# Optimization experiments

Hardware: AMD Instinct MI355X
Metric: run time of the kernel (lower is better)

The kernel has to match this reference:

```python
import jax, jax.numpy as jnp
import numpy as np

B, S, D = 8, 4096, 256
NUM_WINDOW = 8
WIN = S // NUM_WINDOW          # 512
H = 2                          # num_heads
K = D                          # key_dim = d_model per source
DFF = 1024
LN_EPS = 1e-3                  # keras LayerNormalization default epsilon


def _layer_norm(x, g, b):
    mu = jnp.mean(x, axis=-1, keepdims=True)
    var = jnp.mean(jnp.square(x - mu), axis=-1, keepdims=True)
    return (x - mu) * jax.lax.rsqrt(var + LN_EPS) * g + b


def setup_inputs() -> dict:
    key = jax.random.key(0)
    ks = jax.random.split(key, 12)
    s = 0.02
    inp = {
        "x": jax.random.normal(ks[0], (B, S, D), dtype=jnp.float32),
        # MHA projections (keras MultiHeadAttention layout)
        "Wq": jax.random.normal(ks[1], (D, H, K), dtype=jnp.float32) * s,
        "bq": jnp.zeros((H, K), dtype=jnp.float32),
        "Wk": jax.random.normal(ks[2], (D, H, K), dtype=jnp.float32) * s,
        "bk": jnp.zeros((H, K), dtype=jnp.float32),
        "Wv": jax.random.normal(ks[3], (D, H, K), dtype=jnp.float32) * s,
        "bv": jnp.zeros((H, K), dtype=jnp.float32),
        "Wo": jax.random.normal(ks[4], (H, K, D), dtype=jnp.float32) * s,
        "bo": jnp.zeros((D,), dtype=jnp.float32),
        "ln1_g": jnp.ones((D,), dtype=jnp.float32),
        "ln1_b": jnp.zeros((D,), dtype=jnp.float32),
        # FeedForward
        "W1": jax.random.normal(ks[5], (D, DFF), dtype=jnp.float32) * s,
        "b1": jnp.zeros((DFF,), dtype=jnp.float32),
        "W2": jax.random.normal(ks[6], (DFF, D), dtype=jnp.float32) * s,
        "b2": jnp.zeros((D,), dtype=jnp.float32),
        "ln2_g": jnp.ones((D,), dtype=jnp.float32),
        "ln2_b": jnp.zeros((D,), dtype=jnp.float32),
    }
    return inp


def reference(x, Wq, bq, Wk, bk, Wv, bv, Wo, bo, ln1_g, ln1_b,
              W1, b1, W2, b2, ln2_g, ln2_b):
    # --- Localized self-attention: block-diagonal over NUM_WINDOW windows ---
    xw = x.reshape(B, NUM_WINDOW, WIN, D)               # [b, w, s, d]
    q = jnp.einsum('bwsd,dhk->bwshk', xw, Wq) + bq      # [b, w, s, h, k]
    k = jnp.einsum('bwsd,dhk->bwshk', xw, Wk) + bk
    v = jnp.einsum('bwsd,dhk->bwshk', xw, Wv) + bv
    scores = jnp.einsum('bwshk,bwthk->bwhst', q, k) / jnp.sqrt(
        jnp.asarray(K, dtype=x.dtype))                  # [b, w, h, s, t]
    attn = jax.nn.softmax(scores, axis=-1)
    ctx = jnp.einsum('bwhst,bwthk->bwshk', attn, v)     # [b, w, s, h, k]
    attn_out = jnp.einsum('bwshk,hkd->bwsd', ctx, Wo) + bo
    attn_out = attn_out.reshape(B, S, D)                # concat over windows
    x = _layer_norm(x + attn_out, ln1_g, ln1_b)
    # --- FeedForward (dropout inactive at inference) ---
    h = jax.nn.relu(x @ W1 + b1)
    ff = h @ W2 + b2
    return _layer_norm(x + ff, ln2_g, ln2_b)
```

## Files before the change

### kernel.cpp

```cpp
#include <hip/hip_runtime.h>

typedef unsigned short u16;
typedef short short8 __attribute__((ext_vector_type(8)));
typedef float f32x4 __attribute__((ext_vector_type(4)));

#define AS1C const __attribute__((address_space(1))) void*
#define AS3P __attribute__((address_space(3))) void*

__device__ __forceinline__ u16 f2b(float f) {
  unsigned u = __float_as_uint(f);
  return (u16)((u + 0x7fffu + ((u >> 16) & 1u)) >> 16);
}
__device__ __forceinline__ float b2f(u16 h) {
  return __uint_as_float((unsigned)h << 16);
}

#define BB 8
#define SS 4096
#define DD 256
#define MTOK (BB*SS)

#define OFF_WQKVT  ((size_t)0)
#define OFF_WOT    ((size_t)786432)
#define OFF_W1T    ((size_t)1048576)
#define OFF_W2T    ((size_t)1572864)
#define OFF_BQKV   ((size_t)2097152)
#define OFF_XB     ((size_t)2103296)
#define OFF_QKV    ((size_t)18880512)
#define OFF_YB     ((size_t)52434944)
#define OFF_HB     ((size_t)69212160)
#define OFF_VT     ((size_t)119543808)
#define OFF_CTX    ((size_t)153098240)

__global__ __launch_bounds__(256) void cast_x_kernel(const float* __restrict__ x,
                                                     u16* __restrict__ xb) {
  size_t i = ((size_t)blockIdx.x * 256 + threadIdx.x) * 4;
  float4 v = *(const float4*)(x + i);
  ushort4 o;
  o.x = f2b(v.x); o.y = f2b(v.y); o.z = f2b(v.z); o.w = f2b(v.w);
  *(ushort4*)(xb + i) = o;
}

__global__ __launch_bounds__(256) void prep_w_kernel(
    const float* __restrict__ Wq, const float* __restrict__ Wk, const float* __restrict__ Wv,
    const float* __restrict__ Wo, const float* __restrict__ W1, const float* __restrict__ W2,
    const float* __restrict__ bq, const float* __restrict__ bk, const float* __restrict__ bv,
    u16* __restrict__ wqkvt, u16* __restrict__ wot, u16* __restrict__ w1t,
    u16* __restrict__ w2t, float* __restrict__ bqkv)
{
  for (int i = blockIdx.x * 256 + threadIdx.x; i < 1050112; i += 1024 * 256) {
    if (i < 393216) {
      int n = i >> 8, d = i & 255;
      const float* W = (n < 512) ? Wq : (n < 1024) ? Wk : Wv;
      int nn = n & 511;
      wqkvt[i] = f2b(W[d * 512 + nn]);
    } else if (i < 524288) {
      int j = i - 393216;
      int dout = j >> 9, hk = j & 511;
      wot[j] = f2b(Wo[hk * 256 + dout]);
    } else if (i < 786432) {
      int j = i - 524288;
      int f = j >> 8, d = j & 255;
      w1t[j] = f2b(W1[d * 1024 + f]);
    } else if (i < 1048576) {
      int j = i - 786432;
      int d = j >> 10, f = j & 1023;
      w2t[j] = f2b(W2[f * 256 + d]);
    } else {
      int n = i - 1048576;
      bqkv[n] = (n < 512) ? bq[n] : (n < 1024) ? bk[n - 512] : bv[n - 1024];
    }
  }
}

__global__ __launch_bounds__(256) void gemm_nres(
    const u16* __restrict__ A, const u16* __restrict__ BT,
    const float* __restrict__ bias, u16* __restrict__ C,
    u16* __restrict__ vt, int N, int vbase, int relu)
{
  __shared__ __align__(16) u16 lds[16384];
  const int tid = threadIdx.x, lane = tid & 63, wid = tid >> 6;
  const int ln = lane & 15, quad = lane >> 4;
  const int pn = blockIdx.x >> 5;
  const int mg = blockIdx.x & 31;
  const int wno = (wid >> 1) << 5;
  const int wmo = (wid & 1) << 4;
  const long mbase = (long)mg << 10;
  const int nb = pn << 6;
  const u16* Bp = BT + (size_t)nb * 256;
  const u16* Ap = A + (size_t)mbase * 256;

#pragma unroll
  for (int p = 0; p < 8; p++) {
    const int s = p * 256 + tid;
    const int row = s >> 5, pc = s & 31;
    const int c = pc ^ (row & 31);
    __builtin_amdgcn_global_load_lds(
        (AS1C)(Bp + (size_t)row * 256 + c * 8), (AS3P)(lds + s * 8), 16, 0, 0);
  }
  __syncthreads();
  short8 breg[2][8];
#pragma unroll
  for (int j = 0; j < 2; j++) {
    const int row = wno + j * 16 + ln;
#pragma unroll
    for (int ks = 0; ks < 8; ks++)
      breg[j][ks] = *(const short8*)(lds + row * 256 + (((ks << 2) + quad) ^ (row & 31)) * 8);
  }
  __syncthreads();

#pragma unroll
  for (int p = 0; p < 4; p++) {
    const int s = p * 256 + tid;
    const int row = s >> 5, pc = s & 31;
    const int c = pc ^ (row & 31);
    __builtin_amdgcn_global_load_lds(
        (AS1C)(Ap + (size_t)row * 256 + c * 8), (AS3P)(lds + s * 8), 16, 0, 0);
  }

  for (int it = 0; it < 32; it++) {
    const int cur = it & 1;
    const u16* Ab = lds + cur * 8192;
    __syncthreads();
    if (it + 1 < 32) {
      const u16* An = Ap + (size_t)(it + 1) * 32 * 256;
      u16* Ax = lds + (cur ^ 1) * 8192;
#pragma unroll
      for (int p = 0; p < 4; p++) {
        const int s = p * 256 + tid;
        const int row = s >> 5, pc = s & 31;
        const int c = pc ^ (row & 31);
        __builtin_amdgcn_global_load_lds(
            (AS1C)(An + (size_t)row * 256 + c * 8), (AS3P)(Ax + s * 8), 16, 0, 0);
      }
    }
    f32x4 acc[2];
    acc[0] = (f32x4){0.f, 0.f, 0.f, 0.f};
    acc[1] = (f32x4){0.f, 0.f, 0.f, 0.f};
    const int r0 = wmo + ln;
#pragma unroll
    for (int ks = 0; ks < 8; ks++) {
      const short8 a0 = *(const short8*)(Ab + r0 * 256 + (((ks << 2) + quad) ^ (r0 & 31)) * 8);
      acc[0] = __builtin_amdgcn_mfma_f32_16x16x32_bf16(breg[0][ks], a0, acc[0], 0, 0, 0);
      acc[1] = __builtin_amdgcn_mfma_f32_16x16x32_bf16(breg[1][ks], a0, acc[1], 0, 0, 0);
    }
    const long m = mbase + it * 32 + wmo + ln;
    if (nb < vbase) {
#pragma unroll
      for (int j = 0; j < 2; j++) {
        const int n0 = nb + wno + j * 16 + quad * 4;
        f32x4 v = acc[j];
        const float4 b4 = *(const float4*)(bias + n0);
        v[0] += b4.x; v[1] += b4.y; v[2] += b4.z; v[3] += b4.w;
        if (relu) {
#pragma unroll
          for (int r = 0; r < 4; r++) v[r] = fmaxf(v[r], 0.f);
        }
        ushort4 ob;
        ob.x = f2b(v[0]); ob.y = f2b(v[1]); ob.z = f2b(v[2]); ob.w = f2b(v[3]);
        *(ushort4*)(C + (size_t)m * N + n0) = ob;
      }
    } else {
      const int bw = (int)(m >> 9), t = (int)(m & 511);
#pragma unroll
      for (int j = 0; j < 2; j++) {
        const int n0 = nb + wno + j * 16 + quad * 4;
        const int rel = n0 - vbase;
        const int h = rel >> 8, k0 = rel & 255;
        u16* vp = vt + (size_t)(bw * 2 + h) * 131072 + (size_t)k0 * 512 + t;
        const float4 b4 = *(const float4*)(bias + n0);
        vp[0]    = f2b(acc[j][0] + b4.x);
        vp[512]  = f2b(acc[j][1] + b4.y);
        vp[1024] = f2b(acc[j][2] + b4.z);
        vp[1536] = f2b(acc[j][3] + b4.w);
      }
    }
  }
}

__global__ __launch_bounds__(512, 4) void attn_fused(const u16* __restrict__ qkv,
                                                     const u16* __restrict__ vt,
                                                     u16* __restrict__ ctx)
{
  __shared__ __align__(16) u16 lds[35328];
  const int tid = threadIdx.x, lane = tid & 63, wid = tid >> 6;
  const int ln = lane & 15, quad = lane >> 4;
  const int bat = blockIdx.x & 127, mt = blockIdx.x >> 7;
  const int bw = bat >> 1, h = bat & 1;
  const u16* Qb = qkv + (size_t)bw * 786432 + (size_t)h * 256 + (size_t)(mt * 64) * 1536;
  const u16* Kb = qkv + (size_t)bw * 786432 + 512 + (size_t)h * 256;
  const u16* Vb = vt + (size_t)bat * 131072;
  const int wn = wid * 64;
  const int wno = wid * 32;
  u16* Pbuf = lds;
  float* red1 = (float*)(lds + 33280);
  float* red2 = red1 + 512;

  const u16* qp[4];
  const u16* kp[4];
#pragma unroll
  for (int i = 0; i < 4; i++) qp[i] = Qb + (size_t)(i * 16 + ln) * 1536 + quad * 8;
#pragma unroll
  for (int j = 0; j < 4; j++) kp[j] = Kb + (size_t)(wn + j * 16 + ln) * 1536 + quad * 8;

  f32x4 acc[4][4];
#pragma unroll
  for (int i = 0; i < 4; i++)
#pragma unroll
    for (int j = 0; j < 4; j++) acc[i][j] = (f32x4){0.f, 0.f, 0.f, 0.f};

#pragma unroll
  for (int ki = 0; ki < 8; ki++) {
    const int kt = ki * 32;
    short8 a[4], b[4];
#pragma unroll
    for (int i = 0; i < 4; i++) a[i] = *(const short8*)(qp[i] + kt);
#pragma unroll
    for (int j = 0; j < 4; j++) b[j] = *(const short8*)(kp[j] + kt);
    __builtin_amdgcn_s_setprio(1);
#pragma unroll
    for (int i = 0; i < 4; i++)
#pragma unroll
      for (int j = 0; j < 4; j++)
        acc[i][j] = __builtin_amdgcn_mfma_f32_16x16x32_bf16(b[j], a[i], acc[i][j], 0, 0, 0);
    __builtin_amdgcn_s_setprio(0);
  }

  float rowmax[4], rowsum[4];
#pragma unroll
  for (int i = 0; i < 4; i++) {
    float m = -1e30f;
#pragma unroll
    for (int j = 0; j < 4; j++)
#pragma unroll
      for (int r = 0; r < 4; r++) m = fmaxf(m, acc[i][j][r]);
    m = fmaxf(m, __shfl_xor(m, 16));
    m = fmaxf(m, __shfl_xor(m, 32));
    if (quad == 0) red1[wid * 64 + i * 16 + ln] = m;
  }
  __syncthreads();
#pragma unroll
  for (int i = 0; i < 4; i++) {
    float m = -1e30f;
#pragma unroll
    for (int w = 0; w < 8; w++) m = fmaxf(m, red1[w * 64 + i * 16 + ln]);
    rowmax[i] = m;
  }
#pragma unroll
  for (int i = 0; i < 4; i++) {
    float s = 0.f;
#pragma unroll
    for (int j = 0; j < 4; j++)
#pragma unroll
      for (int r = 0; r < 4; r++) {
        const float e = __expf((acc[i][j][r] - rowmax[i]) * 0.0625f);
        acc[i][j][r] = e; s += e;
      }
    s += __shfl_xor(s, 16);
    s += __shfl_xor(s, 32);
    if (quad == 0) red2[wid * 64 + i * 16 + ln] = s;
  }
  __syncthreads();
#pragma unroll
  for (int i = 0; i < 4; i++) {
    float s = 0.f;
#pragma unroll
    for (int w = 0; w < 8; w++) s += red2[w * 64 + i * 16 + ln];
    rowsum[i] = 1.f / s;
  }

  short8 vC[2][2], vN[2][2];
#pragma unroll
  for (int j = 0; j < 2; j++) {
    const int kV = wno + j * 16 + ln;
#pragma unroll
    for (int ks = 0; ks < 2; ks++)
      vC[j][ks] = *(const short8*)(Vb + (size_t)kV * 512 + (ks * 4 + quad) * 8);
  }

#pragma unroll
  for (int i = 0; i < 4; i++)
#pragma unroll
    for (int j = 0; j < 4; j++) {
      ushort4 pb;
      pb.x = f2b(acc[i][j][0] * rowsum[i]);
      pb.y = f2b(acc[i][j][1] * rowsum[i]);
      pb.z = f2b(acc[i][j][2] * rowsum[i]);
      pb.w = f2b(acc[i][j][3] * rowsum[i]);
      *(ushort4*)(Pbuf + (i * 16 + ln) * 520 + wn + j * 16 + quad * 4) = pb;
    }
  __syncthreads();

  f32x4 o[4][2];
#pragma unroll
  for (int i = 0; i < 4; i++) {
    o[i][0] = (f32x4){0.f, 0.f, 0.f, 0.f};
    o[i][1] = (f32x4){0.f, 0.f, 0.f, 0.f};
  }

#pragma unroll
  for (int c = 0; c < 8; c++) {
    if (c < 7) {
#pragma unroll
      for (int j = 0; j < 2; j++) {
        const int kV = wno + j * 16 + ln;
#pragma unroll
        for (int ks = 0; ks < 2; ks++)
          vN[j][ks] = *(const short8*)(Vb + (size_t)kV * 512 + (c + 1) * 64 + (ks * 4 + quad) * 8);
      }
    }
    __builtin_amdgcn_s_setprio(1);
#pragma unroll
    for (int ks = 0; ks < 2; ks++) {
      short8 ap[4];
#pragma unroll
      for (int i = 0; i < 4; i++)
        ap[i] = *(const short8*)(Pbuf + (i * 16 + ln) * 520 + c * 64 + ks * 32 + quad * 8);
#pragma unroll
      for (int j = 0; j < 2; j++)
#pragma unroll
        for (int i = 0; i < 4; i++)
          o[i][j] = __builtin_amdgcn_mfma_f32_16x16x32_bf16(vC[j][ks], ap[i], o[i][j], 0, 0, 0);
    }
    __builtin_amdgcn_s_setprio(0);
#pragma unroll
    for (int j = 0; j < 2; j++)
#pragma unroll
      for (int ks = 0; ks < 2; ks++) vC[j][ks] = vN[j][ks];
  }

  const size_t tokr0 = (size_t)bw * 512 + mt * 64;
#pragma unroll
  for (int i = 0; i < 4; i++) {
    const size_t row = tokr0 + i * 16 + ln;
#pragma unroll
    for (int j = 0; j < 2; j++) {
      const int col = h * 256 + wno + j * 16 + quad * 4;
      ushort4 ob;
      ob.x = f2b(o[i][j][0]); ob.y = f2b(o[i][j][1]);
      ob.z = f2b(o[i][j][2]); ob.w = f2b(o[i][j][3]);
      *(ushort4*)(ctx + row * 512 + col) = ob;
    }
  }
}

__global__ __launch_bounds__(256) void gemm_ln(
    const u16* __restrict__ A, const u16* __restrict__ BT,
    const float* __restrict__ bias, const u16* __restrict__ residb,
    const float* __restrict__ g, const float* __restrict__ beta,
    float* __restrict__ yout, u16* __restrict__ ybout, int K)
{
  __shared__ __align__(16) u16 As[2][2048];
  __shared__ __align__(16) u16 Bs[2][8192];
  __shared__ float redS[4][64], redQ[4][64];
  const int tid = threadIdx.x, lane = tid & 63, wid = tid >> 6;
  const int ln = lane & 15, quad = lane >> 4;
  const long bm = (long)blockIdx.x * 64;
  const int wn = wid * 64;
  const u16* Ab = A + (size_t)bm * K;
  const int nk = K >> 5;

  f32x4 acc[4][4];
#pragma unroll
  for (int i = 0; i < 4; i++)
#pragma unroll
    for (int j = 0; j < 4; j++) acc[i][j] = (f32x4){0.f, 0.f, 0.f, 0.f};

  {
    const int row = tid >> 2, c = tid & 3;
    __builtin_amdgcn_global_load_lds(
        (AS1C)(Ab + (size_t)row * K + c * 8), (AS3P)(&As[0][0] + tid * 8), 16, 0, 0);
#pragma unroll
    for (int p = 0; p < 4; p++) {
      const int s = p * 256 + tid;
      const int br = s >> 2, bc = s & 3;
      __builtin_amdgcn_global_load_lds(
          (AS1C)(BT + (size_t)br * K + bc * 8), (AS3P)(&Bs[0][0] + s * 8), 16, 0, 0);
    }
  }

  for (int kti = 0; kti < nk; kti++) {
    const int cur = kti & 1;
    __syncthreads();
    if (kti + 1 < nk) {
      const int kt = (kti + 1) * 32, nxt = cur ^ 1;
      const int row = tid >> 2, c = tid & 3;
      __builtin_amdgcn_global_load_lds(
          (AS1C)(Ab + (size_t)row * K + kt + c * 8), (AS3P)(&As[nxt][0] + tid * 8), 16, 0, 0);
#pragma unroll
      for (int p = 0; p < 4; p++) {
        const int s = p * 256 + tid;
        const int br = s >> 2, bc = s & 3;
        __builtin_amdgcn_global_load_lds(
            (AS1C)(BT + (size_t)br * K + kt + bc * 8), (AS3P)(&Bs[nxt][0] + s * 8), 16, 0, 0);
      }
    }
    short8 a[4], b[4];
#pragma unroll
    for (int i = 0; i < 4; i++) a[i] = *(const short8*)(&As[cur][0] + (i * 16 + ln) * 32 + quad * 8);
#pragma unroll
    for (int j = 0; j < 4; j++) b[j] = *(const short8*)(&Bs[cur][0] + (wn + j * 16 + ln) * 32 + quad * 8);
    __builtin_amdgcn_s_setprio(1);
#pragma unroll
    for (int i = 0; i < 4; i++)
#pragma unroll
      for (int j = 0; j < 4; j++)
        acc[i][j] = __builtin_amdgcn_mfma_f32_16x16x32_bf16(b[j], a[i], acc[i][j], 0, 0, 0);
    __builtin_amdgcn_s_setprio(0);
  }

#pragma unroll
  for (int i = 0; i < 4; i++) {
    const long gm = bm + i * 16 + ln;
    float s = 0.f, q = 0.f;
#pragma unroll
    for (int j = 0; j < 4; j++) {
      const int n0 = wn + j * 16 + quad * 4;
      const float4 b4 = *(const float4*)(bias + n0);
      const ushort4 r4 = *(const ushort4*)(residb + (size_t)gm * 256 + n0);
      acc[i][j][0] += b4.x + b2f(r4.x);
      acc[i][j][1] += b4.y + b2f(r4.y);
      acc[i][j][2] += b4.z + b2f(r4.z);
      acc[i][j][3] += b4.w + b2f(r4.w);
#pragma unroll
      for (int r = 0; r < 4; r++) { s += acc[i][j][r]; q += acc[i][j][r] * acc[i][j][r]; }
    }
    s += __shfl_xor(s, 16); s += __shfl_xor(s, 32);
    q += __shfl_xor(q, 16); q += __shfl_xor(q, 32);
    if (quad == 0) { redS[wid][i * 16 + ln] = s; redQ[wid][i * 16 + ln] = q; }
  }
  __syncthreads();
#pragma unroll
  for (int i = 0; i < 4; i++) {
    const long gm = bm + i * 16 + ln;
    float s = 0.f, q = 0.f;
#pragma unroll
    for (int w = 0; w < 4; w++) { s += redS[w][i * 16 + ln]; q += redQ[w][i * 16 + ln]; }
    const float mu = s * (1.f / 256.f);
    const float inv = rsqrtf(q * (1.f / 256.f) - mu * mu + 1e-3f);
#pragma unroll
    for (int j = 0; j < 4; j++) {
      const int n0 = wn + j * 16 + quad * 4;
      const float4 gg = *(const float4*)(g + n0);
      const float4 bb = *(const float4*)(beta + n0);
      float o0 = (acc[i][j][0] - mu) * inv * gg.x + bb.x;
      float o1 = (acc[i][j][1] - mu) * inv * gg.y + bb.y;
      float o2 = (acc[i][j][2] - mu) * inv * gg.z + bb.z;
      float o3 = (acc[i][j][3] - mu) * inv * gg.w + bb.w;
      const size_t off = (size_t)gm * 256 + n0;
      if (yout) {
        float4 o4; o4.x = o0; o4.y = o1; o4.z = o2; o4.w = o3;
        *(float4*)(yout + off) = o4;
      }
      if (ybout) {
        ushort4 ob;
        ob.x = f2b(o0); ob.y = f2b(o1); ob.z = f2b(o2); ob.w = f2b(o3);
        *(ushort4*)(ybout + off) = ob;
      }
    }
  }
}

extern "C" void kernel_launch(void* const* d_in, const int* in_sizes, int n_in,
                              void* d_out, int out_size, void* d_ws, size_t ws_size,
                              hipStream_t stream) {
  (void)in_sizes; (void)n_in; (void)out_size; (void)ws_size;
  const float* x    = (const float*)d_in[0];
  const float* Wq   = (const float*)d_in[1];
  const float* bq   = (const float*)d_in[2];
  const float* Wk   = (const float*)d_in[3];
  const float* bk   = (const float*)d_in[4];
  const float* Wv   = (const float*)d_in[5];
  const float* bv   = (const float*)d_in[6];
  const float* Wo   = (const float*)d_in[7];
  const float* bo   = (const float*)d_in[8];
  const float* ln1g = (const float*)d_in[9];
  const float* ln1b = (const float*)d_in[10];
  const float* W1   = (const float*)d_in[11];
  const float* b1   = (const float*)d_in[12];
  const float* W2   = (const float*)d_in[13];
  const float* b2   = (const float*)d_in[14];
  const float* ln2g = (const float*)d_in[15];
  const float* ln2b = (const float*)d_in[16];
  float* out = (float*)d_out;

  char* ws = (char*)d_ws;
  u16*   WQKVT = (u16*)(ws + OFF_WQKVT);
  u16*   WOT   = (u16*)(ws + OFF_WOT);
  u16*   W1T   = (u16*)(ws + OFF_W1T);
  u16*   W2T   = (u16*)(ws + OFF_W2T);
  float* BQKV  = (float*)(ws + OFF_BQKV);
  u16*   XB    = (u16*)(ws + OFF_XB);
  u16*   QKV   = (u16*)(ws + OFF_QKV);
  u16*   YB    = (u16*)(ws + OFF_YB);
  u16*   HB    = (u16*)(ws + OFF_HB);
  u16*   VT    = (u16*)(ws + OFF_VT);
  u16*   CTX   = (u16*)(ws + OFF_CTX);

  cast_x_kernel<<<8192, 256, 0, stream>>>(x, XB);
  prep_w_kernel<<<1024, 256, 0, stream>>>(Wq, Wk, Wv, Wo, W1, W2, bq, bk, bv,
                                          WQKVT, WOT, W1T, W2T, BQKV);
  gemm_nres<<<768, 256, 0, stream>>>(XB, WQKVT, BQKV, QKV, VT, 1536, 1024, 0);
  attn_fused<<<1024, 512, 0, stream>>>(QKV, VT, CTX);
  gemm_ln<<<512, 256, 0, stream>>>(CTX, WOT, bo, XB, ln1g, ln1b, nullptr, YB, 512);
  gemm_nres<<<512, 256, 0, stream>>>(YB, W1T, b1, HB, nullptr, 1024, 1 << 30, 1);
  gemm_ln<<<512, 256, 0, stream>>>(HB, W2T, b2, YB, ln2g, ln2b, out, nullptr, 1024);
}
```

Before: 367.9 us.

## Stage Q, K and V through swizzled LDS and stream P chunks per warp

Result: no change. 368.7 us (+0.2%).

```diff
diff --git a/kernel.cpp b/kernel.cpp
--- a/kernel.cpp
+++ b/kernel.cpp
@@ -182,7 +182,7 @@
                                                      const u16* __restrict__ vt,
                                                      u16* __restrict__ ctx)
 {
-  __shared__ __align__(16) u16 lds[35328];
+  __shared__ __align__(16) u16 lds[34816];
   const int tid = threadIdx.x, lane = tid & 63, wid = tid >> 6;
   const int ln = lane & 15, quad = lane >> 4;
   const int bat = blockIdx.x & 127, mt = blockIdx.x >> 7;
@@ -192,16 +192,35 @@
   const u16* Vb = vt + (size_t)bat * 131072;
   const int wn = wid * 64;
   const int wno = wid * 32;
-  u16* Pbuf = lds;
-  float* red1 = (float*)(lds + 33280);
+  u16* Qs = lds;
+  u16* kbuf = lds + 16384 + wid * 2048;
+  float* red1 = (float*)(lds + 32768);
   float* red2 = red1 + 512;
-
-  const u16* qp[4];
-  const u16* kp[4];
-#pragma unroll
-  for (int i = 0; i < 4; i++) qp[i] = Qb + (size_t)(i * 16 + ln) * 1536 + quad * 8;
-#pragma unroll
-  for (int j = 0; j < 4; j++) kp[j] = Kb + (size_t)(wn + j * 16 + ln) * 1536 + quad * 8;
+  u16* Pb0 = lds;
+  u16* Pb1 = lds + 4608;
+  u16* vbuf = lds + 16384 + wid * 2048;
+
+#pragma unroll
+  for (int p = 0; p < 4; p++) {
+    const int s = p * 512 + tid;
+    const int r = s >> 5, cc = s & 31;
+    const int c = cc ^ (r & 31);
+    __builtin_amdgcn_global_load_lds(
+        (AS1C)(Qb + (size_t)r * 1536 + c * 8), (AS3P)(Qs + s * 8), 16, 0, 0);
+  }
+
+  const u16* Kg = Kb + (size_t)(wn + lane) * 1536;
+  const int ksw = (lane >> 2) & 3;
+  const int krd = (ln >> 2) & 3;
+  short8 kx[4];
+#pragma unroll
+  for (int c = 0; c < 4; c++) kx[c] = *(const short8*)(Kg + c * 8);
+
+  __syncthreads();
+
+#pragma unroll
+  for (int c = 0; c < 4; c++)
+    *(short8*)(kbuf + (lane * 4 + (c ^ ksw)) * 8) = kx[c];
 
   f32x4 acc[4][4];
 #pragma unroll
@@ -209,14 +228,21 @@
 #pragma unroll
     for (int j = 0; j < 4; j++) acc[i][j] = (f32x4){0.f, 0.f, 0.f, 0.f};
 
-#pragma unroll
   for (int ki = 0; ki < 8; ki++) {
-    const int kt = ki * 32;
+    if (ki < 7) {
+#pragma unroll
+      for (int c = 0; c < 4; c++)
+        kx[c] = *(const short8*)(Kg + (ki + 1) * 32 + c * 8);
+    }
     short8 a[4], b[4];
 #pragma unroll
-    for (int i = 0; i < 4; i++) a[i] = *(const short8*)(qp[i] + kt);
-#pragma unroll
-    for (int j = 0; j < 4; j++) b[j] = *(const short8*)(kp[j] + kt);
+    for (int i = 0; i < 4; i++) {
+      const int r = i * 16 + ln;
+      a[i] = *(const short8*)(Qs + (r * 32 + ((ki * 4 + quad) ^ (r & 31))) * 8);
+    }
+#pragma unroll
+    for (int j = 0; j < 4; j++)
+      b[j] = *(const short8*)(kbuf + ((j * 16 + ln) * 4 + (quad ^ krd)) * 8);
     __builtin_amdgcn_s_setprio(1);
 #pragma unroll
     for (int i = 0; i < 4; i++)
@@ -224,6 +250,11 @@
       for (int j = 0; j < 4; j++)
         acc[i][j] = __builtin_amdgcn_mfma_f32_16x16x32_bf16(b[j], a[i], acc[i][j], 0, 0, 0);
     __builtin_amdgcn_s_setprio(0);
+    if (ki < 7) {
+#pragma unroll
+      for (int c = 0; c < 4; c++)
+        *(short8*)(kbuf + (lane * 4 + (c ^ ksw)) * 8) = kx[c];
+    }
   }
 
   float rowmax[4], rowsum[4];
@@ -246,6 +277,14 @@
     for (int w = 0; w < 8; w++) m = fmaxf(m, red1[w * 64 + i * 16 + ln]);
     rowmax[i] = m;
   }
+
+  const int rv = lane & 31, so = lane >> 5;
+  const int vsw = rv & 7;
+  const u16* Vg = Vb + (size_t)(wno + rv) * 512;
+  short8 vx[4];
+#pragma unroll
+  for (int p = 0; p < 4; p++) vx[p] = *(const short8*)(Vg + (so + 2 * p) * 8);
+
 #pragma unroll
   for (int i = 0; i < 4; i++) {
     float s = 0.f;
@@ -269,26 +308,27 @@
     rowsum[i] = 1.f / s;
   }
 
-  short8 vC[2][2], vN[2][2];
-#pragma unroll
-  for (int j = 0; j < 2; j++) {
-    const int kV = wno + j * 16 + ln;
-#pragma unroll
-    for (int ks = 0; ks < 2; ks++)
-      vC[j][ks] = *(const short8*)(Vb + (size_t)kV * 512 + (ks * 4 + quad) * 8);
-  }
-
+  ushort4 pb[4][4];
 #pragma unroll
   for (int i = 0; i < 4; i++)
 #pragma unroll
     for (int j = 0; j < 4; j++) {
-      ushort4 pb;
-      pb.x = f2b(acc[i][j][0] * rowsum[i]);
-      pb.y = f2b(acc[i][j][1] * rowsum[i]);
-      pb.z = f2b(acc[i][j][2] * rowsum[i]);
-      pb.w = f2b(acc[i][j][3] * rowsum[i]);
-      *(ushort4*)(Pbuf + (i * 16 + ln) * 520 + wn + j * 16 + quad * 4) = pb;
-    }
+      pb[i][j].x = f2b(acc[i][j][0] * rowsum[i]);
+      pb[i][j].y = f2b(acc[i][j][1] * rowsum[i]);
+      pb[i][j].z = f2b(acc[i][j][2] * rowsum[i]);
+      pb[i][j].w = f2b(acc[i][j][3] * rowsum[i]);
+    }
+
+#pragma unroll
+  for (int p = 0; p < 4; p++)
+    *(short8*)(vbuf + (rv * 8 + ((so + 2 * p) ^ vsw)) * 8) = vx[p];
+  if (wid == 0) {
+#pragma unroll
+    for (int i = 0; i < 4; i++)
+#pragma unroll
+      for (int j = 0; j < 4; j++)
+        *(ushort4*)(Pb0 + (i * 16 + ln) * 72 + j * 16 + quad * 4) = pb[i][j];
+  }
   __syncthreads();
 
   f32x4 o[4][2];
@@ -298,35 +338,44 @@
     o[i][1] = (f32x4){0.f, 0.f, 0.f, 0.f};
   }
 
-#pragma unroll
   for (int c = 0; c < 8; c++) {
     if (c < 7) {
 #pragma unroll
-      for (int j = 0; j < 2; j++) {
-        const int kV = wno + j * 16 + ln;
-#pragma unroll
-        for (int ks = 0; ks < 2; ks++)
-          vN[j][ks] = *(const short8*)(Vb + (size_t)kV * 512 + (c + 1) * 64 + (ks * 4 + quad) * 8);
-      }
-    }
+      for (int p = 0; p < 4; p++)
+        vx[p] = *(const short8*)(Vg + (c + 1) * 64 + (so + 2 * p) * 8);
+      if (wid == c + 1) {
+        u16* Pn = ((c + 1) & 1) ? Pb1 : Pb0;
+#pragma unroll
+        for (int i = 0; i < 4; i++)
+#pragma unroll
+          for (int j = 0; j < 4; j++)
+            *(ushort4*)(Pn + (i * 16 + ln) * 72 + j * 16 + quad * 4) = pb[i][j];
+      }
+    }
+    const u16* Pc = (c & 1) ? Pb1 : Pb0;
     __builtin_amdgcn_s_setprio(1);
 #pragma unroll
     for (int ks = 0; ks < 2; ks++) {
       short8 ap[4];
 #pragma unroll
       for (int i = 0; i < 4; i++)
-        ap[i] = *(const short8*)(Pbuf + (i * 16 + ln) * 520 + c * 64 + ks * 32 + quad * 8);
-#pragma unroll
-      for (int j = 0; j < 2; j++)
+        ap[i] = *(const short8*)(Pc + (i * 16 + ln) * 72 + ks * 32 + quad * 8);
+#pragma unroll
+      for (int j = 0; j < 2; j++) {
+        const int rr = j * 16 + ln;
+        const short8 bv = *(const short8*)(vbuf + (rr * 8 + ((ks * 4 + quad) ^ (ln & 7))) * 8);
 #pragma unroll
         for (int i = 0; i < 4; i++)
-          o[i][j] = __builtin_amdgcn_mfma_f32_16x16x32_bf16(vC[j][ks], ap[i], o[i][j], 0, 0, 0);
+          o[i][j] = __builtin_amdgcn_mfma_f32_16x16x32_bf16(bv, ap[i], o[i][j], 0, 0, 0);
+      }
     }
     __builtin_amdgcn_s_setprio(0);
-#pragma unroll
-    for (int j = 0; j < 2; j++)
-#pragma unroll
-      for (int ks = 0; ks < 2; ks++) vC[j][ks] = vN[j][ks];
+    if (c < 7) {
+#pragma unroll
+      for (int p = 0; p < 4; p++)
+        *(short8*)(vbuf + (rv * 8 + ((so + 2 * p) ^ vsw)) * 8) = vx[p];
+      __syncthreads();
+    }
   }
 
   const size_t tokr0 = (size_t)bw * 512 + mt * 64;
```
